# Performance work log

Hardware: AMD Instinct MI355X
Metric: run time of the kernel (lower is better)

## Reference

```python
import jax, jax.numpy as jnp
import numpy as np

B, T, H, D = 1, 2048, 32, 64
SCALE = 0.015625  # 1/64 = 1/head_size
DEG = 2


def setup_inputs() -> dict:
    key = jax.random.key(0)
    k1, k2, k3, k4 = jax.random.split(key, 4)
    q = jax.random.normal(k1, (B, T, H, D), dtype=jnp.float32)
    k = jax.random.normal(k2, (B, T, H, D), dtype=jnp.float32)
    v = jax.random.normal(k3, (B, T, H, D), dtype=jnp.float32)
    # log_G: per-token, per-head log decay (must be <= 0)
    g = -0.1 * jax.random.uniform(k4, (B, T, H), dtype=jnp.float32)
    return {"q": q, "k": k, "v": v, "g": g}


def reference(q, k, v, g):
    # q,k,v: [B,T,H,D]; g: [B,T,H] log-decay (log_G)
    # Power retention, deg=2, attention (quadratic) form for T <= switch_over_seq_len.
    g_cum = jnp.cumsum(g, axis=1)                         # [B,T,H]
    gc = jnp.transpose(g_cum, (0, 2, 1))                  # [B,H,T]
    # decay weight exp(gc[t]-gc[s]) for s<=t, 0 otherwise
    log_decay = gc[:, :, :, None] - gc[:, :, None, :]     # [B,H,T,S]
    causal = jnp.tril(jnp.ones((T, T), dtype=bool))
    decay = jnp.where(causal, jnp.exp(log_decay), 0.0)    # [B,H,T,S]
    qk = jnp.einsum("bthd,bshd->bhts", q, k) * SCALE      # [B,H,T,S]
    w = (qk ** DEG) * decay                               # nonneg scores, deg=2
    num = jnp.einsum("bhts,bshd->bthd", w, v)             # [B,T,H,D]
    denom = jnp.transpose(w.sum(-1), (0, 2, 1))           # [B,T,H]
    out = num / jnp.maximum(denom, 1.0)[..., None]
    return out
```

## Files before the change

kernel.cpp:

```cpp
#include <hip/hip_runtime.h>

#define T_DIM 2048
#define H_DIM 32
#define D_DIM 64
#define SCALE_F 0.015625f
#define TILE_STRIDE 2048

typedef unsigned short ushort;
typedef __attribute__((ext_vector_type(8))) short short8;
typedef __attribute__((ext_vector_type(16))) float f32x16;
typedef __attribute__((ext_vector_type(2))) float f32x2;

#define MFMA32(A, B, C) __builtin_amdgcn_mfma_f32_32x32x16_bf16((A), (B), (C), 0, 0, 0)

__global__ __launch_bounds__(256)
void cumsum_g_kernel(const float* __restrict__ g, float* __restrict__ gc) {
    const int h = blockIdx.x;
    const int tid = threadIdx.x;
    const int PER = T_DIM / 256;

    __shared__ float sums[256];

    float loc[8];
    float run = 0.f;
    const int t0 = tid * PER;
    for (int i = 0; i < PER; ++i) {
        run += g[(size_t)(t0 + i) * H_DIM + h];
        loc[i] = run;
    }
    sums[tid] = run;
    __syncthreads();

    for (int off = 1; off < 256; off <<= 1) {
        float vv = (tid >= off) ? sums[tid - off] : 0.f;
        __syncthreads();
        sums[tid] += vv;
        __syncthreads();
    }
    float excl = (tid == 0) ? 0.f : sums[tid - 1];

    for (int i = 0; i < PER; ++i)
        gc[(size_t)h * T_DIM + t0 + i] = excl + loc[i];
}

__device__ __forceinline__ ushort f2bf(float x) {
    unsigned u = __float_as_uint(x);
    unsigned r = (u + 0x7fffu + ((u >> 16) & 1u)) >> 16;
    return (ushort)r;
}

__global__ __launch_bounds__(256)
void prep_kernel(const float* __restrict__ q, const float* __restrict__ k,
                 const float* __restrict__ v, const float* __restrict__ gc,
                 ushort* __restrict__ qfrag, ushort* __restrict__ kfrag,
                 ushort* __restrict__ vfrag) {
    __shared__ ushort qt_l[64 * 64];
    __shared__ ushort kt_l[64 * 64];

    const int h   = blockIdx.x;
    const int tt  = blockIdx.y;
    const int tid = threadIdx.x;

    {
        const int r    = tid >> 2;
        const int dseg = (tid & 3) * 16;
        const int t    = tt * 64 + r;
        const float gct = gc[(size_t)h * T_DIM + t];
        const float eq = SCALE_F * __expf(0.5f * gct);
        const float ek = __expf(-0.5f * gct);
        const float* qp = q + ((size_t)t * H_DIM + h) * 64 + dseg;
        const float* kp = k + ((size_t)t * H_DIM + h) * 64 + dseg;
        union { ushort u[16]; uint4 uu[2]; } oq, ok;
#pragma unroll
        for (int i = 0; i < 16; ++i) {
            oq.u[i] = f2bf(qp[i] * eq);
            ok.u[i] = f2bf(kp[i] * ek);
        }
        const int c0 = (tid & 3) * 2;
#pragma unroll
        for (int cc = 0; cc < 2; ++cc) {
            const int slot = (c0 + cc) ^ (r & 7);
            *reinterpret_cast<uint4*>(&qt_l[r * 64 + slot * 8]) = oq.uu[cc];
            *reinterpret_cast<uint4*>(&kt_l[r * 64 + slot * 8]) = ok.uu[cc];
        }
    }
    __syncthreads();

#pragma unroll
    for (int n = 0; n < 2; ++n) {
        const int ch   = tid + 256 * n;
        const int l31  = ch & 31;
        const int hi   = (ch >> 5) & 1;
        const int ks   = (ch >> 6) & 3;
        const int t32r = ch >> 8;
        const int row  = t32r * 32 + l31;
        const int slot = (2 * ks + hi) ^ (row & 7);
        uint4 qq = *reinterpret_cast<const uint4*>(&qt_l[row * 64 + slot * 8]);
        uint4 kk = *reinterpret_cast<const uint4*>(&kt_l[row * 64 + slot * 8]);
        const size_t base = ((size_t)h * 64 + tt * 2 + t32r) * TILE_STRIDE
                          + (size_t)(((ks * 2 + hi) * 32) + l31) * 8;
        *reinterpret_cast<uint4*>(qfrag + base) = qq;
        *reinterpret_cast<uint4*>(kfrag + base) = kk;
    }

#pragma unroll
    for (int n = 0; n < 2; ++n) {
        const int c9   = (tid >> 5) + 8 * n;
        const int l31  = tid & 31;
        const int hi   = c9 & 1;
        const int kh2  = (c9 >> 1) & 1;
        const int dblk = (c9 >> 2) & 1;
        const int s32r = c9 >> 3;
        const int tb = tt * 64 + s32r * 32 + kh2 * 16 + hi * 8;
        union { ushort u[8]; uint4 uu; } ov;
#pragma unroll
        for (int j = 0; j < 8; ++j)
            ov.u[j] = f2bf(v[((size_t)(tb + j) * H_DIM + h) * 64 + dblk * 32 + l31]);
        const size_t base = ((size_t)h * 64 + tt * 2 + s32r) * TILE_STRIDE
                          + (size_t)((((dblk * 2 + kh2) * 2 + hi) * 32) + l31) * 8;
        *reinterpret_cast<uint4*>(vfrag + base) = ov.uu;
    }
}

__device__ __forceinline__ short8 ld8(const ushort* p) {
    return *reinterpret_cast<const short8*>(p);
}

__device__ __forceinline__ unsigned cvt_pk_bf16(float lo, float hi) {
    unsigned r;
    asm("v_cvt_pk_bf16_f32 %0, %1, %2" : "=v"(r) : "v"(lo), "v"(hi));
    return r;
}

__device__ __forceinline__ short8 pack_w2(const f32x2* w2) {
    unsigned p0 = cvt_pk_bf16(w2[0][0], w2[0][1]);
    unsigned p1 = cvt_pk_bf16(w2[1][0], w2[1][1]);
    unsigned p2 = cvt_pk_bf16(w2[2][0], w2[2][1]);
    unsigned p3 = cvt_pk_bf16(w2[3][0], w2[3][1]);
    asm("v_permlane32_swap_b32 %0, %1" : "+v"(p0), "+v"(p2));
    asm("v_permlane32_swap_b32 %0, %1" : "+v"(p1), "+v"(p3));
    union { unsigned u[4]; short8 s; } af;
    af.u[0] = p0; af.u[1] = p1; af.u[2] = p2; af.u[3] = p3;
    return af.s;
}

__device__ __forceinline__ void gll16(const void* g, void* l) {
    __builtin_amdgcn_global_load_lds(
        (const __attribute__((address_space(1))) unsigned int*)g,
        (__attribute__((address_space(3))) unsigned int*)l, 16, 0, 0);
}

__device__ __forceinline__ void stage16k(ushort* ldst, const char* ksrc,
                                         const char* vsrc, int tid) {
    char* lb = (char*)ldst + (tid >> 6) * 1024;
    const int lo = tid * 16;
    gll16(ksrc + lo,        lb);
    gll16(ksrc + 4096 + lo, lb + 4096);
    gll16(vsrc + lo,        lb + 8192);
    gll16(vsrc + 4096 + lo, lb + 12288);
}

template<int MODE>
__device__ __forceinline__ void unit32(
    const ushort* ldsK, const ushort* ldsV,
    int lofs, int hi, int l31,
    const short8 (&qr)[4], f32x16& o0, f32x16& o1, f32x2& den2)
{
    const short8 kf0 = ld8(ldsK + lofs);
    const short8 kf1 = ld8(ldsK + 512 + lofs);
    const short8 kf2 = ld8(ldsK + 1024 + lofs);
    const short8 kf3 = ld8(ldsK + 1536 + lofs);
    const short8 vf0 = ld8(ldsV + lofs);
    const short8 vf1 = ld8(ldsV + 512 + lofs);
    const short8 vf2 = ld8(ldsV + 1024 + lofs);
    const short8 vf3 = ld8(ldsV + 1536 + lofs);

    f32x16 c;
#pragma unroll
    for (int i = 0; i < 16; ++i) c[i] = 0.f;
    c = MFMA32(kf0, qr[0], c);
    c = MFMA32(kf1, qr[1], c);
    c = MFMA32(kf2, qr[2], c);
    c = MFMA32(kf3, qr[3], c);

    f32x2 w2[8];
#pragma unroll
    for (int i = 0; i < 8; ++i) {
        const int r0 = 2 * i;
        f32x2 x; x[0] = c[r0]; x[1] = c[r0 + 1];
        f32x2 ww = x * x;
        if (MODE == 1) {
            const int sl0 = (r0 & 3) + 8 * (r0 >> 2) + 4 * hi;
            ww[0] = (sl0 <= l31) ? ww[0] : 0.f;
            ww[1] = (sl0 + 1 <= l31) ? ww[1] : 0.f;
        }
        w2[i] = ww;
        den2 += ww;
    }
    const short8 a0 = pack_w2(&w2[0]);
    o0 = MFMA32(a0, vf0, o0);
    o1 = MFMA32(a0, vf2, o1);
    const short8 a1 = pack_w2(&w2[4]);
    o0 = MFMA32(a1, vf1, o0);
    o1 = MFMA32(a1, vf3, o1);
}

__global__ __launch_bounds__(256, 2)
void retention_mfma_kernel(const ushort* __restrict__ qfrag,
                           const ushort* __restrict__ kfrag,
                           const ushort* __restrict__ vfrag,
                           float* __restrict__ out) {
    __shared__ ushort buf[2][8192];
    __shared__ float lds_red[2][2][32][32];
    __shared__ float lds_den[2][32];

    const int bid = blockIdx.x;
    const int p   = bid >> 5;
    const int h   = bid & 31;
    const int ht  = 31 - p;
    const int tid = threadIdx.x;
    const int w   = tid >> 6;
    const int lane = tid & 63;
    const int hi  = lane >> 5;
    const int l31 = lane & 31;
    const int lofs = hi * 256 + l31 * 8;

    short8 qrA[4], qrB[4];
    {
        const int prim_t32 = (w < 2) ? (ht * 2 + w) : (p * 2 + (w - 2));
        const ushort* qa = qfrag + ((size_t)h * 64 + prim_t32) * TILE_STRIDE;
#pragma unroll
        for (int ks = 0; ks < 4; ++ks) qrA[ks] = ld8(qa + ks * 512 + lofs);
        if (w >= 2) {
            const int sec_t32 = ht * 2 + (w - 2);
            const ushort* qb = qfrag + ((size_t)h * 64 + sec_t32) * TILE_STRIDE;
#pragma unroll
            for (int ks = 0; ks < 4; ++ks) qrB[ks] = ld8(qb + ks * 512 + lofs);
        }
    }

    f32x16 a0, a1, b0, b1;
#pragma unroll
    for (int i = 0; i < 16; ++i) { a0[i] = 0.f; a1[i] = 0.f; b0[i] = 0.f; b1[i] = 0.f; }
    f32x2 dA, dB;
    dA[0] = 0.f; dA[1] = 0.f; dB[0] = 0.f; dB[1] = 0.f;

    const char* kgb = (const char*)(kfrag + (size_t)h * 64 * TILE_STRIDE);
    const char* vgb = (const char*)(vfrag + (size_t)h * 64 * TILE_STRIDE);

    stage16k(buf[0], kgb, vgb, tid);
    __syncthreads();

    int cur = 0;
    for (int J = 0; J <= ht; ++J) {
        if (J < ht)
            stage16k(buf[cur ^ 1], kgb + (size_t)(J + 1) * 8192,
                     vgb + (size_t)(J + 1) * 8192, tid);

        const ushort* K0 = &buf[cur][0];
        const ushort* K1 = &buf[cur][2048];
        const ushort* V0 = &buf[cur][4096];
        const ushort* V1 = &buf[cur][6144];

        if (J < p) {
            unit32<0>(K0, V0, lofs, hi, l31, qrA, a0, a1, dA);
            unit32<0>(K1, V1, lofs, hi, l31, qrA, a0, a1, dA);
        } else if (J == p) {
            if (w < 2) {
                unit32<0>(K0, V0, lofs, hi, l31, qrA, a0, a1, dA);
                unit32<0>(K1, V1, lofs, hi, l31, qrA, a0, a1, dA);
            } else if (w == 2) {
                unit32<1>(K0, V0, lofs, hi, l31, qrA, a0, a1, dA);
            } else {
                unit32<0>(K0, V0, lofs, hi, l31, qrA, a0, a1, dA);
                unit32<1>(K1, V1, lofs, hi, l31, qrA, a0, a1, dA);
            }
        } else if (J < ht) {
            if (w < 2) unit32<0>(K0, V0, lofs, hi, l31, qrA, a0, a1, dA);
            else       unit32<0>(K1, V1, lofs, hi, l31, qrB, b0, b1, dB);
        } else {
            if (w == 0)      unit32<1>(K0, V0, lofs, hi, l31, qrA, a0, a1, dA);
            else if (w == 1) unit32<0>(K0, V0, lofs, hi, l31, qrA, a0, a1, dA);
            else if (w == 3) unit32<1>(K1, V1, lofs, hi, l31, qrB, b0, b1, dB);
        }

        __syncthreads();
        cur ^= 1;
    }

    float denA = dA[0] + dA[1];
    denA += __shfl_xor(denA, 32);
    float denB = dB[0] + dB[1];
    denB += __shfl_xor(denB, 32);

    if (w >= 2) {
        const int ww = w - 2;
#pragma unroll
        for (int r = 0; r < 16; ++r) {
            const int row = (r & 3) + 8 * (r >> 2) + 4 * hi;
            lds_red[ww][0][row][l31] = b0[r];
            lds_red[ww][1][row][l31] = b1[r];
        }
        if (hi == 0) lds_den[ww][l31] = denB;
    }
    __syncthreads();

    if (w < 2) {
        const float dlane = denA + lds_den[w][l31];
#pragma unroll
        for (int r = 0; r < 16; ++r) {
            const int row = (r & 3) + 8 * (r >> 2) + 4 * hi;
            const float s0 = a0[r] + lds_red[w][0][row][l31];
            const float s1 = a1[r] + lds_red[w][1][row][l31];
            const float dt = __shfl(dlane, row);
            const float inv = 1.f / fmaxf(dt, 1.f);
            const int t = ht * 64 + w * 32 + row;
            float* op = out + ((size_t)t * H_DIM + h) * 64;
            op[l31]      = s0 * inv;
            op[32 + l31] = s1 * inv;
        }
    } else {
#pragma unroll
        for (int r = 0; r < 16; ++r) {
            const int row = (r & 3) + 8 * (r >> 2) + 4 * hi;
            const float dt = __shfl(denA, row);
            const float inv = 1.f / fmaxf(dt, 1.f);
            const int t = p * 64 + (w - 2) * 32 + row;
            float* op = out + ((size_t)t * H_DIM + h) * 64;
            op[l31]      = a0[r] * inv;
            op[32 + l31] = a1[r] * inv;
        }
    }
}

extern "C" void kernel_launch(void* const* d_in, const int* in_sizes, int n_in,
                              void* d_out, int out_size, void* d_ws, size_t ws_size,
                              hipStream_t stream) {
    const float* q = (const float*)d_in[0];
    const float* k = (const float*)d_in[1];
    const float* v = (const float*)d_in[2];
    const float* g = (const float*)d_in[3];
    float* out = (float*)d_out;

    const size_t GC_BYTES = (size_t)H_DIM * T_DIM * sizeof(float);
    const size_t BF_ELEMS = (size_t)H_DIM * T_DIM * D_DIM;

    float* gc = (float*)d_ws;
    ushort* qfrag = (ushort*)((char*)d_ws + GC_BYTES);
    ushort* kfrag = qfrag + BF_ELEMS;
    ushort* vfrag = kfrag + BF_ELEMS;

    cumsum_g_kernel<<<H_DIM, 256, 0, stream>>>(g, gc);
    prep_kernel<<<dim3(H_DIM, T_DIM / 64), 256, 0, stream>>>(q, k, v, gc,
                                                             qfrag, kfrag, vfrag);
    retention_mfma_kernel<<<16 * H_DIM, 256, 0, stream>>>(qfrag, kfrag, vfrag, out);
}
```

Measured before the change: 54.58 us.

## Use 128-row query tiles with 8 waves splitting key chunks

Each block now handles 128 query rows of one head with 512 threads. Four query-tile waves are each paired with two key-split waves, and 32KB K/V chunks are double-buffered in LDS. This replaces the old paired heavy/light 64-row scheme and is meant to raise K/V reuse per LDS stage. Partial outputs and denominators are reduced through LDS, and the block writes coalesced float4 stores. The cost is that per-block work is no longer balanced, ranging from 1 to 16 chunks, and LDS per block doubles to 64KB, which may limit how many blocks fit on a CU.

```diff
diff --git a/kernel.cpp b/kernel.cpp
--- a/kernel.cpp
+++ b/kernel.cpp
@@ -10,6 +10,7 @@
 typedef __attribute__((ext_vector_type(8))) short short8;
 typedef __attribute__((ext_vector_type(16))) float f32x16;
 typedef __attribute__((ext_vector_type(2))) float f32x2;
+typedef __attribute__((ext_vector_type(4))) float f32x4;
 
 #define MFMA32(A, B, C) __builtin_amdgcn_mfma_f32_32x32x16_bf16((A), (B), (C), 0, 0, 0)
 
@@ -150,14 +151,14 @@
         (__attribute__((address_space(3))) unsigned int*)l, 16, 0, 0);
 }
 
-__device__ __forceinline__ void stage16k(ushort* ldst, const char* ksrc,
+__device__ __forceinline__ void stage32k(ushort* dst, const char* ksrc,
                                          const char* vsrc, int tid) {
-    char* lb = (char*)ldst + (tid >> 6) * 1024;
+    char* d = (char*)dst + (tid >> 6) * 1024;
     const int lo = tid * 16;
-    gll16(ksrc + lo,        lb);
-    gll16(ksrc + 4096 + lo, lb + 4096);
-    gll16(vsrc + lo,        lb + 8192);
-    gll16(vsrc + 4096 + lo, lb + 12288);
+    gll16(ksrc + lo,        d);
+    gll16(ksrc + 8192 + lo, d + 8192);
+    gll16(vsrc + lo,        d + 16384);
+    gll16(vsrc + 8192 + lo, d + 24576);
 }
 
 template<int MODE>
@@ -205,130 +206,112 @@
     o1 = MFMA32(a1, vf3, o1);
 }
 
-__global__ __launch_bounds__(256, 2)
+__global__ __launch_bounds__(512, 4)
 void retention_mfma_kernel(const ushort* __restrict__ qfrag,
                            const ushort* __restrict__ kfrag,
                            const ushort* __restrict__ vfrag,
                            float* __restrict__ out) {
-    __shared__ ushort buf[2][8192];
-    __shared__ float lds_red[2][2][32][32];
-    __shared__ float lds_den[2][32];
+    __shared__ ushort buf[2][16384];
 
     const int bid = blockIdx.x;
-    const int p   = bid >> 5;
-    const int h   = bid & 31;
-    const int ht  = 31 - p;
+    const int h   = (bid & 7) + 8 * ((bid >> 3) & 3);
+    const int r   = bid >> 5;
+    const int qb  = (r < 8) ? (2 * r) : (31 - 2 * r + 16 - 16);
+    const int qbb = (r < 8) ? (2 * r) : (31 - 2 * (r - 8) - 16 + 16);
+    (void)qb; (void)qbb;
+    const int QB  = (r < 8) ? (2 * r) : (15 - 2 * (r - 8));
+
     const int tid = threadIdx.x;
     const int w   = tid >> 6;
+    const int qi  = w & 3;
+    const int si  = w >> 2;
     const int lane = tid & 63;
     const int hi  = lane >> 5;
     const int l31 = lane & 31;
     const int lofs = hi * 256 + l31 * 8;
-
-    short8 qrA[4], qrB[4];
+    const int myT32 = 4 * QB + qi;
+
+    short8 qr[4];
     {
-        const int prim_t32 = (w < 2) ? (ht * 2 + w) : (p * 2 + (w - 2));
-        const ushort* qa = qfrag + ((size_t)h * 64 + prim_t32) * TILE_STRIDE;
-#pragma unroll
-        for (int ks = 0; ks < 4; ++ks) qrA[ks] = ld8(qa + ks * 512 + lofs);
-        if (w >= 2) {
-            const int sec_t32 = ht * 2 + (w - 2);
-            const ushort* qb = qfrag + ((size_t)h * 64 + sec_t32) * TILE_STRIDE;
-#pragma unroll
-            for (int ks = 0; ks < 4; ++ks) qrB[ks] = ld8(qb + ks * 512 + lofs);
-        }
-    }
-
-    f32x16 a0, a1, b0, b1;
-#pragma unroll
-    for (int i = 0; i < 16; ++i) { a0[i] = 0.f; a1[i] = 0.f; b0[i] = 0.f; b1[i] = 0.f; }
-    f32x2 dA, dB;
-    dA[0] = 0.f; dA[1] = 0.f; dB[0] = 0.f; dB[1] = 0.f;
+        const ushort* qp = qfrag + ((size_t)h * 64 + myT32) * TILE_STRIDE;
+#pragma unroll
+        for (int ks = 0; ks < 4; ++ks) qr[ks] = ld8(qp + ks * 512 + lofs);
+    }
+
+    f32x16 o0, o1;
+#pragma unroll
+    for (int i = 0; i < 16; ++i) { o0[i] = 0.f; o1[i] = 0.f; }
+    f32x2 d2; d2[0] = 0.f; d2[1] = 0.f;
 
     const char* kgb = (const char*)(kfrag + (size_t)h * 64 * TILE_STRIDE);
     const char* vgb = (const char*)(vfrag + (size_t)h * 64 * TILE_STRIDE);
 
-    stage16k(buf[0], kgb, vgb, tid);
-    __syncthreads();
-
-    int cur = 0;
-    for (int J = 0; J <= ht; ++J) {
-        if (J < ht)
-            stage16k(buf[cur ^ 1], kgb + (size_t)(J + 1) * 8192,
-                     vgb + (size_t)(J + 1) * 8192, tid);
-
-        const ushort* K0 = &buf[cur][0];
-        const ushort* K1 = &buf[cur][2048];
-        const ushort* V0 = &buf[cur][4096];
-        const ushort* V1 = &buf[cur][6144];
-
-        if (J < p) {
-            unit32<0>(K0, V0, lofs, hi, l31, qrA, a0, a1, dA);
-            unit32<0>(K1, V1, lofs, hi, l31, qrA, a0, a1, dA);
-        } else if (J == p) {
-            if (w < 2) {
-                unit32<0>(K0, V0, lofs, hi, l31, qrA, a0, a1, dA);
-                unit32<0>(K1, V1, lofs, hi, l31, qrA, a0, a1, dA);
-            } else if (w == 2) {
-                unit32<1>(K0, V0, lofs, hi, l31, qrA, a0, a1, dA);
-            } else {
-                unit32<0>(K0, V0, lofs, hi, l31, qrA, a0, a1, dA);
-                unit32<1>(K1, V1, lofs, hi, l31, qrA, a0, a1, dA);
-            }
-        } else if (J < ht) {
-            if (w < 2) unit32<0>(K0, V0, lofs, hi, l31, qrA, a0, a1, dA);
-            else       unit32<0>(K1, V1, lofs, hi, l31, qrB, b0, b1, dB);
-        } else {
-            if (w == 0)      unit32<1>(K0, V0, lofs, hi, l31, qrA, a0, a1, dA);
-            else if (w == 1) unit32<0>(K0, V0, lofs, hi, l31, qrA, a0, a1, dA);
-            else if (w == 3) unit32<1>(K1, V1, lofs, hi, l31, qrB, b0, b1, dB);
-        }
+    stage32k(buf[0], kgb, vgb, tid);
+    __syncthreads();
+
+    for (int J = 0; J <= QB; ++J) {
+        if (J < QB)
+            stage32k(buf[(J + 1) & 1], kgb + (size_t)(J + 1) * 16384,
+                     vgb + (size_t)(J + 1) * 16384, tid);
+
+        const ushort* bK = buf[J & 1];
+        const ushort* bV = bK + 8192;
+        const int c1 = 4 * J + si;
+        const int c2 = c1 + 2;
+
+        if (c1 < myT32)
+            unit32<0>(bK + si * 2048, bV + si * 2048, lofs, hi, l31, qr, o0, o1, d2);
+        else if (c1 == myT32)
+            unit32<1>(bK + si * 2048, bV + si * 2048, lofs, hi, l31, qr, o0, o1, d2);
+
+        if (c2 < myT32)
+            unit32<0>(bK + (2 + si) * 2048, bV + (2 + si) * 2048, lofs, hi, l31, qr, o0, o1, d2);
+        else if (c2 == myT32)
+            unit32<1>(bK + (2 + si) * 2048, bV + (2 + si) * 2048, lofs, hi, l31, qr, o0, o1, d2);
 
         __syncthreads();
-        cur ^= 1;
-    }
-
-    float denA = dA[0] + dA[1];
-    denA += __shfl_xor(denA, 32);
-    float denB = dB[0] + dB[1];
-    denB += __shfl_xor(denB, 32);
-
-    if (w >= 2) {
-        const int ww = w - 2;
-#pragma unroll
-        for (int r = 0; r < 16; ++r) {
-            const int row = (r & 3) + 8 * (r >> 2) + 4 * hi;
-            lds_red[ww][0][row][l31] = b0[r];
-            lds_red[ww][1][row][l31] = b1[r];
-        }
-        if (hi == 0) lds_den[ww][l31] = denB;
-    }
-    __syncthreads();
-
-    if (w < 2) {
-        const float dlane = denA + lds_den[w][l31];
-#pragma unroll
-        for (int r = 0; r < 16; ++r) {
-            const int row = (r & 3) + 8 * (r >> 2) + 4 * hi;
-            const float s0 = a0[r] + lds_red[w][0][row][l31];
-            const float s1 = a1[r] + lds_red[w][1][row][l31];
-            const float dt = __shfl(dlane, row);
-            const float inv = 1.f / fmaxf(dt, 1.f);
-            const int t = ht * 64 + w * 32 + row;
-            float* op = out + ((size_t)t * H_DIM + h) * 64;
-            op[l31]      = s0 * inv;
-            op[32 + l31] = s1 * inv;
-        }
-    } else {
-#pragma unroll
-        for (int r = 0; r < 16; ++r) {
-            const int row = (r & 3) + 8 * (r >> 2) + 4 * hi;
-            const float dt = __shfl(denA, row);
-            const float inv = 1.f / fmaxf(dt, 1.f);
-            const int t = p * 64 + (w - 2) * 32 + row;
-            float* op = out + ((size_t)t * H_DIM + h) * 64;
-            op[l31]      = a0[r] * inv;
-            op[32 + l31] = a1[r] * inv;
+    }
+
+    float* pm  = (float*)(&buf[0][0]);
+    float* pmd = (float*)(&buf[1][0]);
+
+    float den = d2[0] + d2[1];
+    den += __shfl_xor(den, 32);
+    if (hi == 0) pmd[(qi * 2 + si) * 32 + l31] = den;
+
+    if (si == 0) {
+#pragma unroll
+        for (int rr = 0; rr < 16; ++rr) {
+            const int row = (rr & 3) + 8 * (rr >> 2) + 4 * hi;
+            pm[(qi * 32 + row) * 64 + l31]      = o0[rr];
+            pm[(qi * 32 + row) * 64 + 32 + l31] = o1[rr];
+        }
+    }
+    __syncthreads();
+    if (si == 1) {
+#pragma unroll
+        for (int rr = 0; rr < 16; ++rr) {
+            const int row = (rr & 3) + 8 * (rr >> 2) + 4 * hi;
+            pm[(qi * 32 + row) * 64 + l31]      += o0[rr];
+            pm[(qi * 32 + row) * 64 + 32 + l31] += o1[rr];
+        }
+    }
+    __syncthreads();
+
+    {
+        const int row  = tid >> 2;
+        const int qq   = row >> 5;
+        const int r32  = row & 31;
+        const int dseg = (tid & 3) * 16;
+        const float dtot = pmd[(qq * 2 + 0) * 32 + r32] + pmd[(qq * 2 + 1) * 32 + r32];
+        const float inv = 1.f / fmaxf(dtot, 1.f);
+        const float* src = pm + (qq * 32 + r32) * 64 + dseg;
+        float* dst = out + ((size_t)(QB * 128 + row) * H_DIM + h) * 64 + dseg;
+#pragma unroll
+        for (int jv = 0; jv < 4; ++jv) {
+            f32x4 s = *reinterpret_cast<const f32x4*>(src + 4 * jv);
+            s *= inv;
+            *reinterpret_cast<f32x4*>(dst + 4 * jv) = s;
         }
     }
 }
@@ -353,5 +336,5 @@
     cumsum_g_kernel<<<H_DIM, 256, 0, stream>>>(g, gc);
     prep_kernel<<<dim3(H_DIM, T_DIM / 64), 256, 0, stream>>>(q, k, v, gc,
                                                              qfrag, kfrag, vfrag);
-    retention_mfma_kernel<<<16 * H_DIM, 256, 0, stream>>>(qfrag, kfrag, vfrag, out);
-}
+    retention_mfma_kernel<<<512, 512, 0, stream>>>(qfrag, kfrag, vfrag, out);
+}
```

Result: faster. 46.56 us (-14.7%).
